# Performance work log

Hardware: AMD Instinct MI355X
Metric: run time of the kernel (lower is better)

Reference implementation:

```python
import jax, jax.numpy as jnp
import numpy as np

B, C, D, K = 16, 512, 256, 32

def setup_inputs() -> dict:
    key = jax.random.key(0)
    ks = jax.random.split(key, 6)
    s = 1.0 / np.sqrt(D)
    return {
        "h": jax.random.normal(ks[0], (B, C, D), dtype=jnp.float32),
        "topk_idx": jax.random.randint(ks[1], (B, C, K), 0, C, dtype=jnp.int64),
        "topk_scores": jax.random.normal(ks[2], (B, C, K), dtype=jnp.float32),
        "vW": jax.random.normal(ks[3], (D, D), dtype=jnp.float32) * s,
        "vb": jnp.zeros((D,), dtype=jnp.float32),
        "oW": jax.random.normal(ks[4], (D, D), dtype=jnp.float32) * s,
        "ob": jnp.zeros((D,), dtype=jnp.float32),
        "gW": jax.random.normal(ks[5], (2 * D, D), dtype=jnp.float32) * s,
        "gb": jnp.zeros((D,), dtype=jnp.float32),
    }

def reference(h, topk_idx, topk_scores, vW, vb, oW, ob, gW, gb):
    # Gather K neighbor features per (batch, channel): [B, C, K, D]
    b_idx = jnp.arange(h.shape[0])[:, None, None]
    neigh = h[b_idx, topk_idx]                         # [B,C,K,D]
    attn = jax.nn.softmax(topk_scores, axis=-1)        # [B,C,K]
    neigh = jnp.einsum('bckd,de->bcke', neigh, vW) + vb  # v_proj
    agg = jnp.einsum('bck,bckd->bcd', attn, neigh)      # weighted sum
    gate = jax.nn.sigmoid(jnp.concatenate([h, agg], axis=-1) @ gW + gb)
    delta = gate * (agg @ oW + ob)
    return delta
```

## Files before the change

### kernel.cpp

```cpp
#include <hip/hip_runtime.h>
#include <hip/hip_bf16.h>
#include <cstdint>
#include <cstddef>

using short8  = __attribute__((ext_vector_type(8))) short;
using short4v = __attribute__((ext_vector_type(4))) short;
using f32x4   = __attribute__((ext_vector_type(4))) float;

constexpr int NB = 16, NC = 512, ND = 256, NK = 32;
constexpr int ROWS = 32;
constexpr int NROW = NB * NC;
constexpr int NBLK = NROW / ROWS;
constexpr int NTHR = 512;

constexpr int OFF_SW = 32768;
constexpr int OFF_HB = 49152;

constexpr int PVW = 0;
constexpr int POW = 65536;
constexpr int PGW = 131072;
constexpr int PHB = 262144;
constexpr size_t WS_NEED = (size_t)(PHB + NB * 131072) * 2;

static __device__ __forceinline__ unsigned short f2bf(float f) {
    __hip_bfloat16 b = __float2bfloat16(f);
    return *reinterpret_cast<unsigned short*>(&b);
}
static __device__ __forceinline__ short4v f2bf4(float4 v) {
    short4v r;
    r[0] = (short)f2bf(v.x); r[1] = (short)f2bf(v.y);
    r[2] = (short)f2bf(v.z); r[3] = (short)f2bf(v.w);
    return r;
}

__global__ __launch_bounds__(256)
void stk_pack_all(const float* __restrict__ vW, const float* __restrict__ oW,
                  const float* __restrict__ gW, const float* __restrict__ h,
                  unsigned short* __restrict__ ws)
{
    const int blk = blockIdx.x;
    if (blk < 128) {
        const int tid  = blk * 256 + threadIdx.x;
        const int lane = tid & 63;
        const int fl   = tid >> 6;
        const float* src; int nt, ks;
        if (fl < 128)      { src = vW; nt = fl >> 3;         ks = fl & 7;          }
        else if (fl < 256) { src = oW; nt = (fl - 128) >> 3; ks = (fl - 128) & 7;  }
        else               { src = gW; nt = (fl - 256) >> 4; ks = (fl - 256) & 15; }
        const int col = nt * 16 + (lane & 15);
        const int k0  = ks * 32 + (lane >> 4) * 8;
        short8 v;
        #pragma unroll
        for (int j = 0; j < 8; ++j)
            v[j] = (short)f2bf(src[(size_t)(k0 + j) * ND + col]);
        *reinterpret_cast<short8*>(&ws[(size_t)tid * 8]) = v;
    } else {
        const int tid  = (blk - 128) * 256 + threadIdx.x;
        const int lane = tid & 63;
        const int fs   = tid >> 6;
        const int b    = fs >> 8;
        const int ks   = (fs >> 4) & 15;
        const int nt   = fs & 15;
        const float* src = h + (size_t)b * NC * ND;
        const int col = nt * 16 + (lane & 15);
        const int k0  = ks * 32 + (lane >> 4) * 8;
        short8 v;
        #pragma unroll
        for (int j = 0; j < 8; ++j)
            v[j] = (short)f2bf(src[(size_t)(k0 + j) * ND + col]);
        *reinterpret_cast<short8*>(&ws[(size_t)PHB + (size_t)tid * 8]) = v;
    }
}

__global__ __launch_bounds__(512, 2)
void stk_main(const float* __restrict__ h,
              const int*   __restrict__ topk_idx,
              const float* __restrict__ topk_scores,
              const float* __restrict__ vb, const float* __restrict__ ob,
              const float* __restrict__ gb,
              const unsigned short* __restrict__ wsb,
              float* __restrict__ out)
{
    __shared__ __align__(16) char smem[65536];
    float (*s_P)[512] = reinterpret_cast<float(*)[512]>(smem);

    const int t   = threadIdx.x;
    const int bid = (int)blockIdx.x;
    const int swz = ((bid & 7) << 5) + (bid >> 3);
    const int m0  = swz * ROWS;
    const int batch = m0 >> 9;

    const int hr = t >> 4;
    const int hc = (t & 15) * 16;
    short4v hreg[4];
    {
        const float* hrow = h + (size_t)(m0 + hr) * ND + hc;
        #pragma unroll
        for (int u = 0; u < 4; ++u)
            hreg[u] = f2bf4(*reinterpret_cast<const float4*>(hrow + 4 * u));
    }

    {
        float4* p4 = reinterpret_cast<float4*>(smem);
        #pragma unroll
        for (int i = 0; i < 8; ++i)
            p4[t + 512 * i] = float4{0.f, 0.f, 0.f, 0.f};
    }

    const int k  = t & 31;
    const int r0 = t >> 5;
    float att[2]; int id[2];
    #pragma unroll
    for (int half = 0; half < 2; ++half) {
        const int r = r0 + (half << 4);
        const size_t off = (size_t)(m0 + r) * NK + k;
        const float s = topk_scores[off];
        id[half] = topk_idx[off];
        float m = s;
        #pragma unroll
        for (int msk = 16; msk >= 1; msk >>= 1)
            m = fmaxf(m, __shfl_xor(m, msk));
        const float p = __expf(s - m);
        float Z = p;
        #pragma unroll
        for (int msk = 16; msk >= 1; msk >>= 1)
            Z += __shfl_xor(Z, msk);
        att[half] = p / Z;
    }
    __syncthreads();

    atomicAdd(&s_P[r0][id[0]],      att[0]);
    atomicAdd(&s_P[r0 + 16][id[1]], att[1]);
    __syncthreads();

    {
        const int pr  = t >> 4;
        const int pc4 = (t & 15) * 4;
        float4 pch[8];
        #pragma unroll
        for (int u = 0; u < 8; ++u)
            pch[u] = *reinterpret_cast<const float4*>(&s_P[pr][pc4 + 64 * u]);
        __syncthreads();

        const int xr = (pr & 7) << 4;
        #pragma unroll
        for (int u = 0; u < 8; ++u)
            *reinterpret_cast<short4v*>(
                smem + pr * 1024 + (((pc4 + 64 * u) * 2) ^ xr)) = f2bf4(pch[u]);
        const int xh = (hr & 7) << 4;
        #pragma unroll
        for (int u = 0; u < 4; ++u)
            *reinterpret_cast<short4v*>(
                smem + OFF_HB + hr * 512 + (((hc + 4 * u) * 2) ^ xh)) = hreg[u];
    }
    __syncthreads();

    const int lane = t & 63, w = t >> 6;
    const int n0 = 2 * w, lr = lane & 15, lg = lane >> 4;
    const int xa = (lr & 7) << 4;

    {
        f32x4 acc[2][2] = {{f32x4{0,0,0,0}, f32x4{0,0,0,0}},
                           {f32x4{0,0,0,0}, f32x4{0,0,0,0}}};
        const unsigned short* hf = wsb + (size_t)PHB + (size_t)batch * 131072;
        #pragma unroll
        for (int ks = 0; ks < 16; ++ks) {
            short8 b[2];
            #pragma unroll
            for (int n = 0; n < 2; ++n)
                b[n] = *reinterpret_cast<const short8*>(
                    &hf[((size_t)(ks * 16 + n0 + n) * 64 + lane) * 8]);
            const int cb = (ks * 32 + lg * 8) * 2;
            short8 a[2];
            a[0] = *reinterpret_cast<const short8*>(smem + lr * 1024 + (cb ^ xa));
            a[1] = *reinterpret_cast<const short8*>(smem + (16 + lr) * 1024 + (cb ^ xa));
            #pragma unroll
            for (int n = 0; n < 2; ++n) {
                acc[0][n] = __builtin_amdgcn_mfma_f32_16x16x32_bf16(a[0], b[n], acc[0][n], 0, 0, 0);
                acc[1][n] = __builtin_amdgcn_mfma_f32_16x16x32_bf16(a[1], b[n], acc[1][n], 0, 0, 0);
            }
        }
        #pragma unroll
        for (int m = 0; m < 2; ++m)
            #pragma unroll
            for (int n = 0; n < 2; ++n) {
                const int col = (n0 + n) * 16 + lr;
                #pragma unroll
                for (int q = 0; q < 4; ++q) {
                    const int row = m * 16 + 4 * lg + q;
                    *reinterpret_cast<unsigned short*>(
                        smem + OFF_SW + row * 512 + ((col * 2) ^ ((row & 7) << 4))) =
                        f2bf(acc[m][n][q]);
                }
            }
    }
    __syncthreads();

    {
        f32x4 acc[2][2];
        #pragma unroll
        for (int n = 0; n < 2; ++n) {
            const float bv = vb[(n0 + n) * 16 + lr];
            acc[0][n] = f32x4{bv, bv, bv, bv};
            acc[1][n] = f32x4{bv, bv, bv, bv};
        }
        #pragma unroll
        for (int ks = 0; ks < 8; ++ks) {
            short8 b[2];
            #pragma unroll
            for (int n = 0; n < 2; ++n)
                b[n] = *reinterpret_cast<const short8*>(
                    &wsb[(size_t)(PVW + (((n0 + n) * 8 + ks) * 64 + lane) * 8)]);
            const int cb = (ks * 32 + lg * 8) * 2;
            short8 a[2];
            a[0] = *reinterpret_cast<const short8*>(smem + OFF_SW + lr * 512 + (cb ^ xa));
            a[1] = *reinterpret_cast<const short8*>(smem + OFF_SW + (16 + lr) * 512 + (cb ^ xa));
            #pragma unroll
            for (int n = 0; n < 2; ++n) {
                acc[0][n] = __builtin_amdgcn_mfma_f32_16x16x32_bf16(a[0], b[n], acc[0][n], 0, 0, 0);
                acc[1][n] = __builtin_amdgcn_mfma_f32_16x16x32_bf16(a[1], b[n], acc[1][n], 0, 0, 0);
            }
        }
        #pragma unroll
        for (int m = 0; m < 2; ++m)
            #pragma unroll
            for (int n = 0; n < 2; ++n) {
                const int col = (n0 + n) * 16 + lr;
                #pragma unroll
                for (int q = 0; q < 4; ++q) {
                    const int row = m * 16 + 4 * lg + q;
                    *reinterpret_cast<unsigned short*>(
                        smem + row * 512 + ((col * 2) ^ ((row & 7) << 4))) =
                        f2bf(acc[m][n][q]);
                }
            }
    }
    __syncthreads();

    {
        f32x4 ao[2][2], ag[2][2];
        #pragma unroll
        for (int n = 0; n < 2; ++n) {
            const float bo = ob[(n0 + n) * 16 + lr];
            const float bg = gb[(n0 + n) * 16 + lr];
            ao[0][n] = f32x4{bo, bo, bo, bo}; ao[1][n] = ao[0][n];
            ag[0][n] = f32x4{bg, bg, bg, bg}; ag[1][n] = ag[0][n];
        }
        #pragma unroll
        for (int ks = 0; ks < 8; ++ks) {
            short8 b_o[2], b_g1[2], b_g2[2];
            #pragma unroll
            for (int n = 0; n < 2; ++n) {
                const int nt = n0 + n;
                b_o[n]  = *reinterpret_cast<const short8*>(
                    &wsb[(size_t)(POW + ((nt * 8 + ks) * 64 + lane) * 8)]);
                b_g1[n] = *reinterpret_cast<const short8*>(
                    &wsb[(size_t)(PGW + ((nt * 16 + ks) * 64 + lane) * 8)]);
                b_g2[n] = *reinterpret_cast<const short8*>(
                    &wsb[(size_t)(PGW + ((nt * 16 + ks + 8) * 64 + lane) * 8)]);
            }
            const int cb = (ks * 32 + lg * 8) * 2;
            short8 aa[2], ah[2];
            aa[0] = *reinterpret_cast<const short8*>(smem + lr * 512 + (cb ^ xa));
            aa[1] = *reinterpret_cast<const short8*>(smem + (16 + lr) * 512 + (cb ^ xa));
            ah[0] = *reinterpret_cast<const short8*>(smem + OFF_HB + lr * 512 + (cb ^ xa));
            ah[1] = *reinterpret_cast<const short8*>(smem + OFF_HB + (16 + lr) * 512 + (cb ^ xa));
            #pragma unroll
            for (int n = 0; n < 2; ++n) {
                #pragma unroll
                for (int m = 0; m < 2; ++m) {
                    ao[m][n] = __builtin_amdgcn_mfma_f32_16x16x32_bf16(aa[m], b_o[n],  ao[m][n], 0, 0, 0);
                    ag[m][n] = __builtin_amdgcn_mfma_f32_16x16x32_bf16(ah[m], b_g1[n], ag[m][n], 0, 0, 0);
                    ag[m][n] = __builtin_amdgcn_mfma_f32_16x16x32_bf16(aa[m], b_g2[n], ag[m][n], 0, 0, 0);
                }
            }
        }
        #pragma unroll
        for (int m = 0; m < 2; ++m)
            #pragma unroll
            for (int n = 0; n < 2; ++n) {
                const int col = (n0 + n) * 16 + lr;
                #pragma unroll
                for (int q = 0; q < 4; ++q) {
                    const int row = m0 + m * 16 + 4 * lg + q;
                    const float g = 1.f / (1.f + __expf(-ag[m][n][q]));
                    out[(size_t)row * ND + col] = g * ao[m][n][q];
                }
            }
    }
}

__global__ __launch_bounds__(512, 2)
void stk_fused(const float* __restrict__ h,
               const int*   __restrict__ topk_idx,
               const float* __restrict__ topk_scores,
               const float* __restrict__ vW, const float* __restrict__ vb,
               const float* __restrict__ oW, const float* __restrict__ ob,
               const float* __restrict__ gW, const float* __restrict__ gb,
               float* __restrict__ out)
{
    __shared__ float s_attn[32][NK];
    __shared__ int   s_idx [32][NK];
    __shared__ float s_wsum[32][ND];
    __shared__ float s_h   [32][ND];
    __shared__ float s_agg [32][ND];

    const int t  = threadIdx.x;
    const int m0 = blockIdx.x * 32;
    const size_t hb = (size_t)(m0 >> 9) * NC * ND;

    {
        const int k  = t & 31;
        const int r0 = t >> 5;
        #pragma unroll
        for (int half = 0; half < 2; ++half) {
            const int r = r0 + (half << 4);
            const size_t off = (size_t)(m0 + r) * NK + k;
            const float s = topk_scores[off];
            const int  id = topk_idx[off];
            float m = s;
            #pragma unroll
            for (int msk = 16; msk >= 1; msk >>= 1) m = fmaxf(m, __shfl_xor(m, msk));
            const float p = __expf(s - m);
            float Z = p;
            #pragma unroll
            for (int msk = 16; msk >= 1; msk >>= 1) Z += __shfl_xor(Z, msk);
            s_attn[r][k] = p / Z;
            s_idx [r][k] = id;
        }
    }
    __syncthreads();

    const int d  = t & 127;
    const int rb = (t >> 7) * 8;

    #pragma unroll
    for (int i = 0; i < 8; ++i) {
        const int r = rb + i;
        const size_t ro = (size_t)(m0 + r) * ND;
        s_h[r][d]       = h[ro + d];
        s_h[r][d + 128] = h[ro + d + 128];
    }
    #pragma unroll 1
    for (int i = 0; i < 8; ++i) {
        const int r = rb + i;
        float a0 = 0.f, a1 = 0.f;
        #pragma unroll 8
        for (int k = 0; k < NK; ++k) {
            const float w  = s_attn[r][k];
            const size_t nb = hb + (size_t)s_idx[r][k] * ND;
            a0 = fmaf(w, h[nb + d],       a0);
            a1 = fmaf(w, h[nb + d + 128], a1);
        }
        s_wsum[r][d]       = a0;
        s_wsum[r][d + 128] = a1;
    }
    __syncthreads();

    float agg0[8], agg1[8];
    {
        const float b0 = vb[d], b1 = vb[d + 128];
        #pragma unroll
        for (int i = 0; i < 8; ++i) { agg0[i] = b0; agg1[i] = b1; }
        for (int e0 = 0; e0 < ND; e0 += 4) {
            float w0[4], w1[4];
            #pragma unroll
            for (int j = 0; j < 4; ++j) {
                w0[j] = vW[(size_t)(e0 + j) * ND + d];
                w1[j] = vW[(size_t)(e0 + j) * ND + d + 128];
            }
            #pragma unroll
            for (int i = 0; i < 8; ++i) {
                const float4 a = *reinterpret_cast<const float4*>(&s_wsum[rb + i][e0]);
                agg0[i] = fmaf(a.x, w0[0], agg0[i]); agg1[i] = fmaf(a.x, w1[0], agg1[i]);
                agg0[i] = fmaf(a.y, w0[1], agg0[i]); agg1[i] = fmaf(a.y, w1[1], agg1[i]);
                agg0[i] = fmaf(a.z, w0[2], agg0[i]); agg1[i] = fmaf(a.z, w1[2], agg1[i]);
                agg0[i] = fmaf(a.w, w0[3], agg0[i]); agg1[i] = fmaf(a.w, w1[3], agg1[i]);
            }
        }
        #pragma unroll
        for (int i = 0; i < 8; ++i) {
            s_agg[rb + i][d]       = agg0[i];
            s_agg[rb + i][d + 128] = agg1[i];
        }
    }
    __syncthreads();

    float o0[8], o1[8], g0[8], g1[8];
    {
        const float obb0 = ob[d], obb1 = ob[d + 128];
        const float gbb0 = gb[d], gbb1 = gb[d + 128];
        #pragma unroll
        for (int i = 0; i < 8; ++i) { o0[i]=obb0; o1[i]=obb1; g0[i]=gbb0; g1[i]=gbb1; }
        for (int e0 = 0; e0 < ND; e0 += 4) {
            float ow0[4], ow1[4], gh0[4], gh1[4], ga0[4], ga1[4];
            #pragma unroll
            for (int j = 0; j < 4; ++j) {
                const size_t er = (size_t)(e0 + j) * ND;
                ow0[j] = oW[er + d];                    ow1[j] = oW[er + d + 128];
                gh0[j] = gW[er + d];                    gh1[j] = gW[er + d + 128];
                ga0[j] = gW[er + (size_t)ND * ND + d];  ga1[j] = gW[er + (size_t)ND * ND + d + 128];
            }
            #pragma unroll
            for (int i = 0; i < 8; ++i) {
                const float4 a  = *reinterpret_cast<const float4*>(&s_agg[rb + i][e0]);
                const float4 hh = *reinterpret_cast<const float4*>(&s_h  [rb + i][e0]);
                o0[i] = fmaf(a.x, ow0[0], o0[i]); o0[i] = fmaf(a.y, ow0[1], o0[i]);
                o0[i] = fmaf(a.z, ow0[2], o0[i]); o0[i] = fmaf(a.w, ow0[3], o0[i]);
                o1[i] = fmaf(a.x, ow1[0], o1[i]); o1[i] = fmaf(a.y, ow1[1], o1[i]);
                o1[i] = fmaf(a.z, ow1[2], o1[i]); o1[i] = fmaf(a.w, ow1[3], o1[i]);
                g0[i] = fmaf(hh.x, gh0[0], g0[i]); g0[i] = fmaf(hh.y, gh0[1], g0[i]);
                g0[i] = fmaf(hh.z, gh0[2], g0[i]); g0[i] = fmaf(hh.w, gh0[3], g0[i]);
                g1[i] = fmaf(hh.x, gh1[0], g1[i]); g1[i] = fmaf(hh.y, gh1[1], g1[i]);
                g1[i] = fmaf(hh.z, gh1[2], g1[i]); g1[i] = fmaf(hh.w, gh1[3], g1[i]);
                g0[i] = fmaf(a.x, ga0[0], g0[i]); g0[i] = fmaf(a.y, ga0[1], g0[i]);
                g0[i] = fmaf(a.z, ga0[2], g0[i]); g0[i] = fmaf(a.w, ga0[3], g0[i]);
                g1[i] = fmaf(a.x, ga1[0], g1[i]); g1[i] = fmaf(a.y, ga1[1], g1[i]);
                g1[i] = fmaf(a.z, ga1[2], g1[i]); g1[i] = fmaf(a.w, ga1[3], g1[i]);
            }
        }
    }
    #pragma unroll
    for (int i = 0; i < 8; ++i) {
        const size_t ro = (size_t)(m0 + rb + i) * ND;
        const float sg0 = 1.f / (1.f + __expf(-g0[i]));
        const float sg1 = 1.f / (1.f + __expf(-g1[i]));
        out[ro + d]       = sg0 * o0[i];
        out[ro + d + 128] = sg1 * o1[i];
    }
}

extern "C" void kernel_launch(void* const* d_in, const int* in_sizes, int n_in,
                              void* d_out, int out_size, void* d_ws, size_t ws_size,
                              hipStream_t stream) {
    const float* h   = (const float*)d_in[0];
    const int*   idx = (const int*)  d_in[1];
    const float* sc  = (const float*)d_in[2];
    const float* vW  = (const float*)d_in[3];
    const float* vb  = (const float*)d_in[4];
    const float* oW  = (const float*)d_in[5];
    const float* ob  = (const float*)d_in[6];
    const float* gW  = (const float*)d_in[7];
    const float* gb  = (const float*)d_in[8];
    float* out = (float*)d_out;

    if (ws_size >= WS_NEED) {
        unsigned short* wsb = (unsigned short*)d_ws;
        stk_pack_all<<<1152, 256, 0, stream>>>(vW, oW, gW, h, wsb);
        stk_main    <<<NBLK, NTHR, 0, stream>>>(h, idx, sc, vb, ob, gb, wsb, out);
    } else {
        stk_fused<<<256, 512, 0, stream>>>(h, idx, sc, vW, vb, oW, ob, gW, gb, out);
    }
}
```

Measured before the change: 29.13 us.

## Prefetch first hf tiles early and move h-gate GEMM into v_proj phase

Issues global loads for the first four k-steps of the per-batch hf operand before the softmax/P-matrix build, so their latency overlaps that phase. Also moves the h-half of the gate GEMM (h @ gW_top) from the final phase into the v_proj phase, which balances MFMA work across phases and shortens the last stage's dependency chain. The cost is higher register pressure from keeping 8 prefetched short8 values and 8 gate accumulators live across phases, which could hurt occupancy under the 2-blocks launch bound.

```diff
diff --git a/kernel.cpp b/kernel.cpp
--- a/kernel.cpp
+++ b/kernel.cpp
@@ -90,6 +90,19 @@
     const int m0  = swz * ROWS;
     const int batch = m0 >> 9;
 
+    const int lane = t & 63, w = t >> 6;
+    const int n0 = 2 * w, lr = lane & 15, lg = lane >> 4;
+    const int xa = (lr & 7) << 4;
+
+    const unsigned short* hf = wsb + (size_t)PHB + (size_t)batch * 131072;
+    short8 pre_b[8];
+    #pragma unroll
+    for (int pk = 0; pk < 4; ++pk)
+        #pragma unroll
+        for (int n = 0; n < 2; ++n)
+            pre_b[pk * 2 + n] = *reinterpret_cast<const short8*>(
+                &hf[((size_t)(pk * 16 + n0 + n) * 64 + lane) * 8]);
+
     const int hr = t >> 4;
     const int hc = (t & 15) * 16;
     short4v hreg[4];
@@ -155,21 +168,21 @@
     }
     __syncthreads();
 
-    const int lane = t & 63, w = t >> 6;
-    const int n0 = 2 * w, lr = lane & 15, lg = lane >> 4;
-    const int xa = (lr & 7) << 4;
-
     {
         f32x4 acc[2][2] = {{f32x4{0,0,0,0}, f32x4{0,0,0,0}},
                            {f32x4{0,0,0,0}, f32x4{0,0,0,0}}};
-        const unsigned short* hf = wsb + (size_t)PHB + (size_t)batch * 131072;
         #pragma unroll
         for (int ks = 0; ks < 16; ++ks) {
             short8 b[2];
-            #pragma unroll
-            for (int n = 0; n < 2; ++n)
-                b[n] = *reinterpret_cast<const short8*>(
-                    &hf[((size_t)(ks * 16 + n0 + n) * 64 + lane) * 8]);
+            if (ks < 4) {
+                b[0] = pre_b[ks * 2];
+                b[1] = pre_b[ks * 2 + 1];
+            } else {
+                #pragma unroll
+                for (int n = 0; n < 2; ++n)
+                    b[n] = *reinterpret_cast<const short8*>(
+                        &hf[((size_t)(ks * 16 + n0 + n) * 64 + lane) * 8]);
+            }
             const int cb = (ks * 32 + lg * 8) * 2;
             short8 a[2];
             a[0] = *reinterpret_cast<const short8*>(smem + lr * 1024 + (cb ^ xa));
@@ -196,6 +209,14 @@
     }
     __syncthreads();
 
+    f32x4 ag[2][2];
+    #pragma unroll
+    for (int n = 0; n < 2; ++n) {
+        const float bg = gb[(n0 + n) * 16 + lr];
+        ag[0][n] = f32x4{bg, bg, bg, bg};
+        ag[1][n] = ag[0][n];
+    }
+
     {
         f32x4 acc[2][2];
         #pragma unroll
@@ -206,19 +227,27 @@
         }
         #pragma unroll
         for (int ks = 0; ks < 8; ++ks) {
-            short8 b[2];
-            #pragma unroll
-            for (int n = 0; n < 2; ++n)
-                b[n] = *reinterpret_cast<const short8*>(
-                    &wsb[(size_t)(PVW + (((n0 + n) * 8 + ks) * 64 + lane) * 8)]);
+            short8 b_v[2], b_g1[2];
+            #pragma unroll
+            for (int n = 0; n < 2; ++n) {
+                const int nt = n0 + n;
+                b_v[n]  = *reinterpret_cast<const short8*>(
+                    &wsb[(size_t)(PVW + ((nt * 8 + ks) * 64 + lane) * 8)]);
+                b_g1[n] = *reinterpret_cast<const short8*>(
+                    &wsb[(size_t)(PGW + ((nt * 16 + ks) * 64 + lane) * 8)]);
+            }
             const int cb = (ks * 32 + lg * 8) * 2;
-            short8 a[2];
-            a[0] = *reinterpret_cast<const short8*>(smem + OFF_SW + lr * 512 + (cb ^ xa));
-            a[1] = *reinterpret_cast<const short8*>(smem + OFF_SW + (16 + lr) * 512 + (cb ^ xa));
-            #pragma unroll
-            for (int n = 0; n < 2; ++n) {
-                acc[0][n] = __builtin_amdgcn_mfma_f32_16x16x32_bf16(a[0], b[n], acc[0][n], 0, 0, 0);
-                acc[1][n] = __builtin_amdgcn_mfma_f32_16x16x32_bf16(a[1], b[n], acc[1][n], 0, 0, 0);
+            short8 a[2], ah[2];
+            a[0]  = *reinterpret_cast<const short8*>(smem + OFF_SW + lr * 512 + (cb ^ xa));
+            a[1]  = *reinterpret_cast<const short8*>(smem + OFF_SW + (16 + lr) * 512 + (cb ^ xa));
+            ah[0] = *reinterpret_cast<const short8*>(smem + OFF_HB + lr * 512 + (cb ^ xa));
+            ah[1] = *reinterpret_cast<const short8*>(smem + OFF_HB + (16 + lr) * 512 + (cb ^ xa));
+            #pragma unroll
+            for (int n = 0; n < 2; ++n) {
+                acc[0][n] = __builtin_amdgcn_mfma_f32_16x16x32_bf16(a[0],  b_v[n],  acc[0][n], 0, 0, 0);
+                acc[1][n] = __builtin_amdgcn_mfma_f32_16x16x32_bf16(a[1],  b_v[n],  acc[1][n], 0, 0, 0);
+                ag[0][n]  = __builtin_amdgcn_mfma_f32_16x16x32_bf16(ah[0], b_g1[n], ag[0][n],  0, 0, 0);
+                ag[1][n]  = __builtin_amdgcn_mfma_f32_16x16x32_bf16(ah[1], b_g1[n], ag[1][n],  0, 0, 0);
             }
         }
         #pragma unroll
@@ -238,39 +267,33 @@
     __syncthreads();
 
     {
-        f32x4 ao[2][2], ag[2][2];
+        f32x4 ao[2][2];
         #pragma unroll
         for (int n = 0; n < 2; ++n) {
             const float bo = ob[(n0 + n) * 16 + lr];
-            const float bg = gb[(n0 + n) * 16 + lr];
-            ao[0][n] = f32x4{bo, bo, bo, bo}; ao[1][n] = ao[0][n];
-            ag[0][n] = f32x4{bg, bg, bg, bg}; ag[1][n] = ag[0][n];
+            ao[0][n] = f32x4{bo, bo, bo, bo};
+            ao[1][n] = ao[0][n];
         }
         #pragma unroll
         for (int ks = 0; ks < 8; ++ks) {
-            short8 b_o[2], b_g1[2], b_g2[2];
+            short8 b_o[2], b_g2[2];
             #pragma unroll
             for (int n = 0; n < 2; ++n) {
                 const int nt = n0 + n;
                 b_o[n]  = *reinterpret_cast<const short8*>(
                     &wsb[(size_t)(POW + ((nt * 8 + ks) * 64 + lane) * 8)]);
-                b_g1[n] = *reinterpret_cast<const short8*>(
-                    &wsb[(size_t)(PGW + ((nt * 16 + ks) * 64 + lane) * 8)]);
                 b_g2[n] = *reinterpret_cast<const short8*>(
                     &wsb[(size_t)(PGW + ((nt * 16 + ks + 8) * 64 + lane) * 8)]);
             }
             const int cb = (ks * 32 + lg * 8) * 2;
-            short8 aa[2], ah[2];
+            short8 aa[2];
             aa[0] = *reinterpret_cast<const short8*>(smem + lr * 512 + (cb ^ xa));
             aa[1] = *reinterpret_cast<const short8*>(smem + (16 + lr) * 512 + (cb ^ xa));
-            ah[0] = *reinterpret_cast<const short8*>(smem + OFF_HB + lr * 512 + (cb ^ xa));
-            ah[1] = *reinterpret_cast<const short8*>(smem + OFF_HB + (16 + lr) * 512 + (cb ^ xa));
             #pragma unroll
             for (int n = 0; n < 2; ++n) {
                 #pragma unroll
                 for (int m = 0; m < 2; ++m) {
                     ao[m][n] = __builtin_amdgcn_mfma_f32_16x16x32_bf16(aa[m], b_o[n],  ao[m][n], 0, 0, 0);
-                    ag[m][n] = __builtin_amdgcn_mfma_f32_16x16x32_bf16(ah[m], b_g1[n], ag[m][n], 0, 0, 0);
                     ag[m][n] = __builtin_amdgcn_mfma_f32_16x16x32_bf16(aa[m], b_g2[n], ag[m][n], 0, 0, 0);
                 }
             }
```

New measurement: 29.09 us. No clear change (-0.2%).

## Halve rows per block to 16 and move h-gate GEMM into v_proj stage

Applied to the files above, without the earlier changes.

Each block now handles 16 rows instead of 32, which halves shared memory to 32KB and raises the launch-bounds occupancy target to 4 blocks per CU. This doubles the grid to 512 blocks and adjusts the swizzle to match. The h·gW1 part of the gate is computed alongside the v_proj MFMA loop so its loads and MFMAs overlap that stage. The cost is that each block reuses the weight fragments it loads from global memory over half as many rows, so total weight traffic through L2 roughly doubles.

```diff
diff --git a/kernel.cpp b/kernel.cpp
--- a/kernel.cpp
+++ b/kernel.cpp
@@ -8,13 +8,13 @@
 using f32x4   = __attribute__((ext_vector_type(4))) float;
 
 constexpr int NB = 16, NC = 512, ND = 256, NK = 32;
-constexpr int ROWS = 32;
+constexpr int ROWS = 16;
 constexpr int NROW = NB * NC;
 constexpr int NBLK = NROW / ROWS;
 constexpr int NTHR = 512;
 
-constexpr int OFF_SW = 32768;
-constexpr int OFF_HB = 49152;
+constexpr int OFF_SW = 16384;
+constexpr int OFF_HB = 24576;
 
 constexpr int PVW = 0;
 constexpr int POW = 65536;
@@ -72,7 +72,7 @@
     }
 }
 
-__global__ __launch_bounds__(512, 2)
+__global__ __launch_bounds__(512, 4)
 void stk_main(const float* __restrict__ h,
               const int*   __restrict__ topk_idx,
               const float* __restrict__ topk_scores,
@@ -81,41 +81,42 @@
               const unsigned short* __restrict__ wsb,
               float* __restrict__ out)
 {
-    __shared__ __align__(16) char smem[65536];
+    __shared__ __align__(16) char smem[32768];
     float (*s_P)[512] = reinterpret_cast<float(*)[512]>(smem);
 
     const int t   = threadIdx.x;
     const int bid = (int)blockIdx.x;
-    const int swz = ((bid & 7) << 5) + (bid >> 3);
+    const int swz = ((bid & 7) << 6) + (bid >> 3);
     const int m0  = swz * ROWS;
     const int batch = m0 >> 9;
 
-    const int hr = t >> 4;
-    const int hc = (t & 15) * 16;
-    short4v hreg[4];
+    const int lane = t & 63, w = t >> 6;
+    const int n0 = 2 * w, lr = lane & 15, lg = lane >> 4;
+    const int xa = (lr & 7) << 4;
+
+    const int hr = t >> 5;
+    const int hc = (t & 31) * 8;
+    short4v hreg[2];
     {
         const float* hrow = h + (size_t)(m0 + hr) * ND + hc;
-        #pragma unroll
-        for (int u = 0; u < 4; ++u)
-            hreg[u] = f2bf4(*reinterpret_cast<const float4*>(hrow + 4 * u));
+        hreg[0] = f2bf4(*reinterpret_cast<const float4*>(hrow));
+        hreg[1] = f2bf4(*reinterpret_cast<const float4*>(hrow + 4));
     }
 
     {
         float4* p4 = reinterpret_cast<float4*>(smem);
         #pragma unroll
-        for (int i = 0; i < 8; ++i)
+        for (int i = 0; i < 4; ++i)
             p4[t + 512 * i] = float4{0.f, 0.f, 0.f, 0.f};
     }
 
-    const int k  = t & 31;
-    const int r0 = t >> 5;
-    float att[2]; int id[2];
-    #pragma unroll
-    for (int half = 0; half < 2; ++half) {
-        const int r = r0 + (half << 4);
+    const int k = t & 31;
+    const int r = t >> 5;
+    float att; int id;
+    {
         const size_t off = (size_t)(m0 + r) * NK + k;
         const float s = topk_scores[off];
-        id[half] = topk_idx[off];
+        id = topk_idx[off];
         float m = s;
         #pragma unroll
         for (int msk = 16; msk >= 1; msk >>= 1)
@@ -125,43 +126,37 @@
         #pragma unroll
         for (int msk = 16; msk >= 1; msk >>= 1)
             Z += __shfl_xor(Z, msk);
-        att[half] = p / Z;
-    }
-    __syncthreads();
-
-    atomicAdd(&s_P[r0][id[0]],      att[0]);
-    atomicAdd(&s_P[r0 + 16][id[1]], att[1]);
-    __syncthreads();
-
-    {
-        const int pr  = t >> 4;
-        const int pc4 = (t & 15) * 4;
-        float4 pch[8];
-        #pragma unroll
-        for (int u = 0; u < 8; ++u)
-            pch[u] = *reinterpret_cast<const float4*>(&s_P[pr][pc4 + 64 * u]);
+        att = p / Z;
+    }
+    __syncthreads();
+
+    atomicAdd(&s_P[r][id], att);
+    __syncthreads();
+
+    {
+        const int pr  = t >> 5;
+        const int pc4 = (t & 31) * 4;
+        float4 pch[4];
+        #pragma unroll
+        for (int u = 0; u < 4; ++u)
+            pch[u] = *reinterpret_cast<const float4*>(&s_P[pr][pc4 + 128 * u]);
         __syncthreads();
 
         const int xr = (pr & 7) << 4;
-        #pragma unroll
-        for (int u = 0; u < 8; ++u)
-            *reinterpret_cast<short4v*>(
-                smem + pr * 1024 + (((pc4 + 64 * u) * 2) ^ xr)) = f2bf4(pch[u]);
-        const int xh = (hr & 7) << 4;
         #pragma unroll
         for (int u = 0; u < 4; ++u)
             *reinterpret_cast<short4v*>(
-                smem + OFF_HB + hr * 512 + (((hc + 4 * u) * 2) ^ xh)) = hreg[u];
-    }
-    __syncthreads();
-
-    const int lane = t & 63, w = t >> 6;
-    const int n0 = 2 * w, lr = lane & 15, lg = lane >> 4;
-    const int xa = (lr & 7) << 4;
-
-    {
-        f32x4 acc[2][2] = {{f32x4{0,0,0,0}, f32x4{0,0,0,0}},
-                           {f32x4{0,0,0,0}, f32x4{0,0,0,0}}};
+                smem + pr * 1024 + (((pc4 + 128 * u) * 2) ^ xr)) = f2bf4(pch[u]);
+        const int xh = (hr & 7) << 4;
+        *reinterpret_cast<short4v*>(
+            smem + OFF_HB + hr * 512 + ((hc * 2) ^ xh)) = hreg[0];
+        *reinterpret_cast<short4v*>(
+            smem + OFF_HB + hr * 512 + (((hc + 4) * 2) ^ xh)) = hreg[1];
+    }
+    __syncthreads();
+
+    {
+        f32x4 acc[2] = {f32x4{0,0,0,0}, f32x4{0,0,0,0}};
         const unsigned short* hf = wsb + (size_t)PHB + (size_t)batch * 131072;
         #pragma unroll
         for (int ks = 0; ks < 16; ++ks) {
@@ -171,122 +166,109 @@
                 b[n] = *reinterpret_cast<const short8*>(
                     &hf[((size_t)(ks * 16 + n0 + n) * 64 + lane) * 8]);
             const int cb = (ks * 32 + lg * 8) * 2;
-            short8 a[2];
-            a[0] = *reinterpret_cast<const short8*>(smem + lr * 1024 + (cb ^ xa));
-            a[1] = *reinterpret_cast<const short8*>(smem + (16 + lr) * 1024 + (cb ^ xa));
-            #pragma unroll
-            for (int n = 0; n < 2; ++n) {
-                acc[0][n] = __builtin_amdgcn_mfma_f32_16x16x32_bf16(a[0], b[n], acc[0][n], 0, 0, 0);
-                acc[1][n] = __builtin_amdgcn_mfma_f32_16x16x32_bf16(a[1], b[n], acc[1][n], 0, 0, 0);
-            }
-        }
-        #pragma unroll
-        for (int m = 0; m < 2; ++m)
-            #pragma unroll
-            for (int n = 0; n < 2; ++n) {
-                const int col = (n0 + n) * 16 + lr;
-                #pragma unroll
-                for (int q = 0; q < 4; ++q) {
-                    const int row = m * 16 + 4 * lg + q;
-                    *reinterpret_cast<unsigned short*>(
-                        smem + OFF_SW + row * 512 + ((col * 2) ^ ((row & 7) << 4))) =
-                        f2bf(acc[m][n][q]);
-                }
-            }
-    }
-    __syncthreads();
-
-    {
-        f32x4 acc[2][2];
+            const short8 a = *reinterpret_cast<const short8*>(smem + lr * 1024 + (cb ^ xa));
+            #pragma unroll
+            for (int n = 0; n < 2; ++n)
+                acc[n] = __builtin_amdgcn_mfma_f32_16x16x32_bf16(a, b[n], acc[n], 0, 0, 0);
+        }
+        #pragma unroll
+        for (int n = 0; n < 2; ++n) {
+            const int col = (n0 + n) * 16 + lr;
+            #pragma unroll
+            for (int q = 0; q < 4; ++q) {
+                const int row = 4 * lg + q;
+                *reinterpret_cast<unsigned short*>(
+                    smem + OFF_SW + row * 512 + ((col * 2) ^ ((row & 7) << 4))) =
+                    f2bf(acc[n][q]);
+            }
+        }
+    }
+    __syncthreads();
+
+    f32x4 ag[2];
+    #pragma unroll
+    for (int n = 0; n < 2; ++n) {
+        const float bg = gb[(n0 + n) * 16 + lr];
+        ag[n] = f32x4{bg, bg, bg, bg};
+    }
+
+    {
+        f32x4 acc[2];
         #pragma unroll
         for (int n = 0; n < 2; ++n) {
             const float bv = vb[(n0 + n) * 16 + lr];
-            acc[0][n] = f32x4{bv, bv, bv, bv};
-            acc[1][n] = f32x4{bv, bv, bv, bv};
+            acc[n] = f32x4{bv, bv, bv, bv};
         }
         #pragma unroll
         for (int ks = 0; ks < 8; ++ks) {
-            short8 b[2];
-            #pragma unroll
-            for (int n = 0; n < 2; ++n)
-                b[n] = *reinterpret_cast<const short8*>(
-                    &wsb[(size_t)(PVW + (((n0 + n) * 8 + ks) * 64 + lane) * 8)]);
+            short8 b_v[2], b_g1[2];
+            #pragma unroll
+            for (int n = 0; n < 2; ++n) {
+                const int nt = n0 + n;
+                b_v[n]  = *reinterpret_cast<const short8*>(
+                    &wsb[(size_t)(PVW + ((nt * 8 + ks) * 64 + lane) * 8)]);
+                b_g1[n] = *reinterpret_cast<const short8*>(
+                    &wsb[(size_t)(PGW + ((nt * 16 + ks) * 64 + lane) * 8)]);
+            }
             const int cb = (ks * 32 + lg * 8) * 2;
-            short8 a[2];
-            a[0] = *reinterpret_cast<const short8*>(smem + OFF_SW + lr * 512 + (cb ^ xa));
-            a[1] = *reinterpret_cast<const short8*>(smem + OFF_SW + (16 + lr) * 512 + (cb ^ xa));
+            const short8 a  = *reinterpret_cast<const short8*>(smem + OFF_SW + lr * 512 + (cb ^ xa));
+            const short8 ah = *reinterpret_cast<const short8*>(smem + OFF_HB + lr * 512 + (cb ^ xa));
             #pragma unroll
             for (int n = 0; n < 2; ++n) {
-                acc[0][n] = __builtin_amdgcn_mfma_f32_16x16x32_bf16(a[0], b[n], acc[0][n], 0, 0, 0);
-                acc[1][n] = __builtin_amdgcn_mfma_f32_16x16x32_bf16(a[1], b[n], acc[1][n], 0, 0, 0);
-            }
-        }
-        #pragma unroll
-        for (int m = 0; m < 2; ++m)
-            #pragma unroll
-            for (int n = 0; n < 2; ++n) {
-                const int col = (n0 + n) * 16 + lr;
-                #pragma unroll
-                for (int q = 0; q < 4; ++q) {
-                    const int row = m * 16 + 4 * lg + q;
-                    *reinterpret_cast<unsigned short*>(
-                        smem + row * 512 + ((col * 2) ^ ((row & 7) << 4))) =
-                        f2bf(acc[m][n][q]);
-                }
-            }
-    }
-    __syncthreads();
-
-    {
-        f32x4 ao[2][2], ag[2][2];
+                acc[n] = __builtin_amdgcn_mfma_f32_16x16x32_bf16(a,  b_v[n],  acc[n], 0, 0, 0);
+                ag[n]  = __builtin_amdgcn_mfma_f32_16x16x32_bf16(ah, b_g1[n], ag[n],  0, 0, 0);
+            }
+        }
+        #pragma unroll
+        for (int n = 0; n < 2; ++n) {
+            const int col = (n0 + n) * 16 + lr;
+            #pragma unroll
+            for (int q = 0; q < 4; ++q) {
+                const int row = 4 * lg + q;
+                *reinterpret_cast<unsigned short*>(
+                    smem + row * 512 + ((col * 2) ^ ((row & 7) << 4))) =
+                    f2bf(acc[n][q]);
+            }
+        }
+    }
+    __syncthreads();
+
+    {
+        f32x4 ao[2];
         #pragma unroll
         for (int n = 0; n < 2; ++n) {
             const float bo = ob[(n0 + n) * 16 + lr];
-            const float bg = gb[(n0 + n) * 16 + lr];
-            ao[0][n] = f32x4{bo, bo, bo, bo}; ao[1][n] = ao[0][n];
-            ag[0][n] = f32x4{bg, bg, bg, bg}; ag[1][n] = ag[0][n];
+            ao[n] = f32x4{bo, bo, bo, bo};
         }
         #pragma unroll
         for (int ks = 0; ks < 8; ++ks) {
-            short8 b_o[2], b_g1[2], b_g2[2];
+            short8 b_o[2], b_g2[2];
             #pragma unroll
             for (int n = 0; n < 2; ++n) {
                 const int nt = n0 + n;
                 b_o[n]  = *reinterpret_cast<const short8*>(
                     &wsb[(size_t)(POW + ((nt * 8 + ks) * 64 + lane) * 8)]);
-                b_g1[n] = *reinterpret_cast<const short8*>(
-                    &wsb[(size_t)(PGW + ((nt * 16 + ks) * 64 + lane) * 8)]);
                 b_g2[n] = *reinterpret_cast<const short8*>(
                     &wsb[(size_t)(PGW + ((nt * 16 + ks + 8) * 64 + lane) * 8)]);
             }
             const int cb = (ks * 32 + lg * 8) * 2;
-            short8 aa[2], ah[2];
-            aa[0] = *reinterpret_cast<const short8*>(smem + lr * 512 + (cb ^ xa));
-            aa[1] = *reinterpret_cast<const short8*>(smem + (16 + lr) * 512 + (cb ^ xa));
-            ah[0] = *reinterpret_cast<const short8*>(smem + OFF_HB + lr * 512 + (cb ^ xa));
-            ah[1] = *reinterpret_cast<const short8*>(smem + OFF_HB + (16 + lr) * 512 + (cb ^ xa));
+            const short8 aa = *reinterpret_cast<const short8*>(smem + lr * 512 + (cb ^ xa));
             #pragma unroll
             for (int n = 0; n < 2; ++n) {
-                #pragma unroll
-                for (int m = 0; m < 2; ++m) {
-                    ao[m][n] = __builtin_amdgcn_mfma_f32_16x16x32_bf16(aa[m], b_o[n],  ao[m][n], 0, 0, 0);
-                    ag[m][n] = __builtin_amdgcn_mfma_f32_16x16x32_bf16(ah[m], b_g1[n], ag[m][n], 0, 0, 0);
-                    ag[m][n] = __builtin_amdgcn_mfma_f32_16x16x32_bf16(aa[m], b_g2[n], ag[m][n], 0, 0, 0);
-                }
-            }
-        }
-        #pragma unroll
-        for (int m = 0; m < 2; ++m)
-            #pragma unroll
-            for (int n = 0; n < 2; ++n) {
-                const int col = (n0 + n) * 16 + lr;
-                #pragma unroll
-                for (int q = 0; q < 4; ++q) {
-                    const int row = m0 + m * 16 + 4 * lg + q;
-                    const float g = 1.f / (1.f + __expf(-ag[m][n][q]));
-                    out[(size_t)row * ND + col] = g * ao[m][n][q];
-                }
-            }
+                ao[n] = __builtin_amdgcn_mfma_f32_16x16x32_bf16(aa, b_o[n],  ao[n], 0, 0, 0);
+                ag[n] = __builtin_amdgcn_mfma_f32_16x16x32_bf16(aa, b_g2[n], ag[n], 0, 0, 0);
+            }
+        }
+        #pragma unroll
+        for (int n = 0; n < 2; ++n) {
+            const int col = (n0 + n) * 16 + lr;
+            #pragma unroll
+            for (int q = 0; q < 4; ++q) {
+                const int row = m0 + 4 * lg + q;
+                const float g = 1.f / (1.f + __expf(-ag[n][q]));
+                out[(size_t)row * ND + col] = g * ao[n][q];
+            }
+        }
     }
 }
 
```

Result: no change. 29.25 us (+0.4%).
